# Optimization experiments

Hardware: AMD Instinct MI355X
Metric: run time of the kernel (lower is better)

Reference implementation:

```python
import jax, jax.numpy as jnp
import numpy as np


def setup_inputs() -> dict:
    key = jax.random.key(0)
    k1, k2 = jax.random.split(key)
    B, C, Tx, Ty, d = 16, 64, 128, 128, 768
    xs = jax.random.normal(k1, (B, Tx, d), dtype=jnp.float32)
    ys = jax.random.normal(k2, (B, C, Ty, d), dtype=jnp.float32)
    return {"xs": xs, "ys": ys}


def reference(xs, ys):
    """UnifiedRetriever HardAttention scoring.

    xs: (B, T_x, d) mention poly-code embeddings
    ys: (B, C, T_y, d) candidate entity poly-code embeddings
    returns: (B, C) scores
    Matches torch: matmul(xs, ys.reshape(B,-1,d).T).reshape(B,Tx,C,Ty).max(-1)[0].sum(1)
    """
    # (B, Tx, C, Ty) dot-product similarity scores
    scores = jnp.einsum("bxd,bcyd->bxcy", xs, ys)
    # max over candidate tokens, sum over mention tokens -> (B, C)
    return scores.max(axis=-1).sum(axis=1)
```

## Files before the change

kernel.cpp:

```cpp
#include <hip/hip_runtime.h>

#define NB 16
#define NC 64
#define TX 128
#define TY 128
#define DD 768
#define BK 32
#define NT (DD / BK)

typedef __bf16 bf16_t;
typedef __bf16 bf16x8 __attribute__((ext_vector_type(8)));
typedef __bf16 bf16x4 __attribute__((ext_vector_type(4)));
typedef float  f32x4  __attribute__((ext_vector_type(4)));

__device__ __forceinline__ unsigned swz(unsigned r, unsigned kb) {
  return r * 64u + ((((kb >> 4) & 3u) ^ ((r >> 1) & 3u)) << 4) + (kb & 15u);
}

__device__ __forceinline__ void cvt_store(void* dst, f32x4 v) {
  bf16x4 q;
  q[0] = (bf16_t)v[0]; q[1] = (bf16_t)v[1]; q[2] = (bf16_t)v[2]; q[3] = (bf16_t)v[3];
  *(bf16x4*)dst = q;
}

__global__ __launch_bounds__(256, 4) void ur_score_kernel(
    const float* __restrict__ xs, const float* __restrict__ ys,
    float* __restrict__ out)
{
  __shared__ char lds[2][2][8192];
  __shared__ float wsum[4];

  const int u  = blockIdx.x;
  const int b  = u & 15;
  const int c  = u >> 4;
  const int bc = b * NC + c;

  const int tid  = threadIdx.x;
  const int lane = tid & 63;
  const int w    = tid >> 6;

  const unsigned r0 = (unsigned)tid >> 3;
  const unsigned j0 = (unsigned)tid & 7u;
  const unsigned soff0 = swz(r0, j0 * 8u);
  const float* Ap = xs + (size_t)b  * TX * DD + r0 * DD + j0 * 4;
  const float* Bp = ys + (size_t)bc * TY * DD + r0 * DD + j0 * 4;

  f32x4 acc[2][8];
  #pragma unroll
  for (int m = 0; m < 2; ++m)
    #pragma unroll
    for (int n = 0; n < 8; ++n)
      #pragma unroll
      for (int k = 0; k < 4; ++k)
        acc[m][n][k] = 0.0f;

  f32x4 pa[4], pb[4];

  #pragma unroll
  for (int i = 0; i < 4; ++i) {
    pa[i] = __builtin_nontemporal_load((const f32x4*)(Ap + i * 32 * DD));
    pb[i] = __builtin_nontemporal_load((const f32x4*)(Bp + i * 32 * DD));
  }
  #pragma unroll
  for (int i = 0; i < 4; ++i) {
    cvt_store(&lds[0][0][soff0 + 2048u * i], pa[i]);
    cvt_store(&lds[0][1][soff0 + 2048u * i], pb[i]);
  }
  #pragma unroll
  for (int i = 0; i < 4; ++i) {
    pa[i] = __builtin_nontemporal_load((const f32x4*)(Ap + BK + i * 32 * DD));
    pb[i] = __builtin_nontemporal_load((const f32x4*)(Bp + BK + i * 32 * DD));
  }
  asm volatile("s_waitcnt lgkmcnt(0)" ::: "memory");
  __builtin_amdgcn_s_barrier();
  asm volatile("" ::: "memory");

  const unsigned kb = ((unsigned)lane >> 4) << 4;
  const unsigned rA = (unsigned)(w * 32 + (lane & 15));
  const unsigned rB = (unsigned)(lane & 15);
  const unsigned aoff = swz(rA, kb);
  const unsigned boff = swz(rB, kb);

  int cur = 0;
  for (int t = 0; t < NT; ++t) {
    if (t + 1 < NT) {
      #pragma unroll
      for (int i = 0; i < 4; ++i) {
        cvt_store(&lds[cur ^ 1][0][soff0 + 2048u * i], pa[i]);
        cvt_store(&lds[cur ^ 1][1][soff0 + 2048u * i], pb[i]);
      }
    }
    if (t + 2 < NT) {
      #pragma unroll
      for (int i = 0; i < 4; ++i) {
        pa[i] = __builtin_nontemporal_load((const f32x4*)(Ap + (t + 2) * BK + i * 32 * DD));
        pb[i] = __builtin_nontemporal_load((const f32x4*)(Bp + (t + 2) * BK + i * 32 * DD));
      }
    }
    bf16x8 af0 = *(const bf16x8*)&lds[cur][0][aoff];
    bf16x8 af1 = *(const bf16x8*)&lds[cur][0][aoff + 1024u];
    bf16x8 bfr[8];
    #pragma unroll
    for (int n = 0; n < 8; ++n)
      bfr[n] = *(const bf16x8*)&lds[cur][1][boff + 1024u * n];
    #pragma unroll
    for (int n = 0; n < 8; ++n)
      acc[0][n] = __builtin_amdgcn_mfma_f32_16x16x32_bf16(af0, bfr[n], acc[0][n], 0, 0, 0);
    #pragma unroll
    for (int n = 0; n < 8; ++n)
      acc[1][n] = __builtin_amdgcn_mfma_f32_16x16x32_bf16(af1, bfr[n], acc[1][n], 0, 0, 0);

    asm volatile("s_waitcnt lgkmcnt(0)" ::: "memory");
    __builtin_amdgcn_s_barrier();
    asm volatile("" ::: "memory");
    cur ^= 1;
  }

  float rm[2][4];
  #pragma unroll
  for (int m = 0; m < 2; ++m)
    #pragma unroll
    for (int i = 0; i < 4; ++i) {
      float v = acc[m][0][i];
      #pragma unroll
      for (int n = 1; n < 8; ++n) v = fmaxf(v, acc[m][n][i]);
      rm[m][i] = v;
    }
  #pragma unroll
  for (int mask = 1; mask < 16; mask <<= 1)
    #pragma unroll
    for (int m = 0; m < 2; ++m)
      #pragma unroll
      for (int i = 0; i < 4; ++i)
        rm[m][i] = fmaxf(rm[m][i], __shfl_xor(rm[m][i], mask, 64));

  float ps = 0.0f;
  #pragma unroll
  for (int m = 0; m < 2; ++m)
    #pragma unroll
    for (int i = 0; i < 4; ++i) ps += rm[m][i];
  ps += __shfl_xor(ps, 16, 64);
  ps += __shfl_xor(ps, 32, 64);

  if (lane == 0) wsum[w] = ps;
  __syncthreads();
  if (tid == 0) out[bc] = wsum[0] + wsum[1] + wsum[2] + wsum[3];
}

extern "C" void kernel_launch(void* const* d_in, const int* in_sizes, int n_in,
                              void* d_out, int out_size, void* d_ws, size_t ws_size,
                              hipStream_t stream) {
  const float* xs = (const float*)d_in[0];
  const float* ys = (const float*)d_in[1];
  float* out = (float*)d_out;
  ur_score_kernel<<<dim3(NB * NC), dim3(256), 0, stream>>>(xs, ys, out);
}
```

Before: 90.45 us.

## Double threads per block to 512 and switch xs loads to cached

Each block now uses 8 waves instead of 4, and each wave computes 16 rows of the 128x128 tile instead of 32. This halves the per-thread global loads and the accumulator registers, aiming for more latency hiding from additional resident waves. The xs loads drop the nontemporal hint so the shared mention embeddings can stay in cache across the 64 candidate blocks. The cost is more threads contending at each barrier, and every wave still reads all 8 B fragments, which raises LDS read traffic per MFMA.

```diff
diff --git a/kernel.cpp b/kernel.cpp
--- a/kernel.cpp
+++ b/kernel.cpp
@@ -23,12 +23,12 @@
   *(bf16x4*)dst = q;
 }
 
-__global__ __launch_bounds__(256, 4) void ur_score_kernel(
+__global__ __launch_bounds__(512, 2) void ur_score_kernel(
     const float* __restrict__ xs, const float* __restrict__ ys,
     float* __restrict__ out)
 {
   __shared__ char lds[2][2][8192];
-  __shared__ float wsum[4];
+  __shared__ float wsum[8];
 
   const int u  = blockIdx.x;
   const int b  = u & 15;
@@ -45,38 +45,36 @@
   const float* Ap = xs + (size_t)b  * TX * DD + r0 * DD + j0 * 4;
   const float* Bp = ys + (size_t)bc * TY * DD + r0 * DD + j0 * 4;
 
-  f32x4 acc[2][8];
+  f32x4 acc[8];
   #pragma unroll
-  for (int m = 0; m < 2; ++m)
+  for (int n = 0; n < 8; ++n)
     #pragma unroll
-    for (int n = 0; n < 8; ++n)
-      #pragma unroll
-      for (int k = 0; k < 4; ++k)
-        acc[m][n][k] = 0.0f;
+    for (int k = 0; k < 4; ++k)
+      acc[n][k] = 0.0f;
 
-  f32x4 pa[4], pb[4];
+  f32x4 pa[2], pb[2];
 
   #pragma unroll
-  for (int i = 0; i < 4; ++i) {
-    pa[i] = __builtin_nontemporal_load((const f32x4*)(Ap + i * 32 * DD));
-    pb[i] = __builtin_nontemporal_load((const f32x4*)(Bp + i * 32 * DD));
+  for (int i = 0; i < 2; ++i) {
+    pa[i] = *(const f32x4*)(Ap + i * 64 * DD);
+    pb[i] = __builtin_nontemporal_load((const f32x4*)(Bp + i * 64 * DD));
   }
   #pragma unroll
-  for (int i = 0; i < 4; ++i) {
-    cvt_store(&lds[0][0][soff0 + 2048u * i], pa[i]);
-    cvt_store(&lds[0][1][soff0 + 2048u * i], pb[i]);
+  for (int i = 0; i < 2; ++i) {
+    cvt_store(&lds[0][0][soff0 + 4096u * i], pa[i]);
+    cvt_store(&lds[0][1][soff0 + 4096u * i], pb[i]);
   }
   #pragma unroll
-  for (int i = 0; i < 4; ++i) {
-    pa[i] = __builtin_nontemporal_load((const f32x4*)(Ap + BK + i * 32 * DD));
-    pb[i] = __builtin_nontemporal_load((const f32x4*)(Bp + BK + i * 32 * DD));
+  for (int i = 0; i < 2; ++i) {
+    pa[i] = *(const f32x4*)(Ap + BK + i * 64 * DD);
+    pb[i] = __builtin_nontemporal_load((const f32x4*)(Bp + BK + i * 64 * DD));
   }
   asm volatile("s_waitcnt lgkmcnt(0)" ::: "memory");
   __builtin_amdgcn_s_barrier();
   asm volatile("" ::: "memory");
 
   const unsigned kb = ((unsigned)lane >> 4) << 4;
-  const unsigned rA = (unsigned)(w * 32 + (lane & 15));
+  const unsigned rA = (unsigned)(w * 16 + (lane & 15));
   const unsigned rB = (unsigned)(lane & 15);
   const unsigned aoff = swz(rA, kb);
   const unsigned boff = swz(rB, kb);
@@ -85,30 +83,26 @@
   for (int t = 0; t < NT; ++t) {
     if (t + 1 < NT) {
       #pragma unroll
-      for (int i = 0; i < 4; ++i) {
-        cvt_store(&lds[cur ^ 1][0][soff0 + 2048u * i], pa[i]);
-        cvt_store(&lds[cur ^ 1][1][soff0 + 2048u * i], pb[i]);
+      for (int i = 0; i < 2; ++i) {
+        cvt_store(&lds[cur ^ 1][0][soff0 + 4096u * i], pa[i]);
+        cvt_store(&lds[cur ^ 1][1][soff0 + 4096u * i], pb[i]);
       }
     }
     if (t + 2 < NT) {
       #pragma unroll
-      for (int i = 0; i < 4; ++i) {
-        pa[i] = __builtin_nontemporal_load((const f32x4*)(Ap + (t + 2) * BK + i * 32 * DD));
-        pb[i] = __builtin_nontemporal_load((const f32x4*)(Bp + (t + 2) * BK + i * 32 * DD));
+      for (int i = 0; i < 2; ++i) {
+        pa[i] = *(const f32x4*)(Ap + (t + 2) * BK + i * 64 * DD);
+        pb[i] = __builtin_nontemporal_load((const f32x4*)(Bp + (t + 2) * BK + i * 64 * DD));
       }
     }
-    bf16x8 af0 = *(const bf16x8*)&lds[cur][0][aoff];
-    bf16x8 af1 = *(const bf16x8*)&lds[cur][0][aoff + 1024u];
+    bf16x8 af = *(const bf16x8*)&lds[cur][0][aoff];
     bf16x8 bfr[8];
     #pragma unroll
     for (int n = 0; n < 8; ++n)
       bfr[n] = *(const bf16x8*)&lds[cur][1][boff + 1024u * n];
     #pragma unroll
     for (int n = 0; n < 8; ++n)
-      acc[0][n] = __builtin_amdgcn_mfma_f32_16x16x32_bf16(af0, bfr[n], acc[0][n], 0, 0, 0);
-    #pragma unroll
-    for (int n = 0; n < 8; ++n)
-      acc[1][n] = __builtin_amdgcn_mfma_f32_16x16x32_bf16(af1, bfr[n], acc[1][n], 0, 0, 0);
+      acc[n] = __builtin_amdgcn_mfma_f32_16x16x32_bf16(af, bfr[n], acc[n], 0, 0, 0);
 
     asm volatile("s_waitcnt lgkmcnt(0)" ::: "memory");
     __builtin_amdgcn_s_barrier();
@@ -116,35 +110,32 @@
     cur ^= 1;
   }
 
-  float rm[2][4];
+  float rm[4];
   #pragma unroll
-  for (int m = 0; m < 2; ++m)
+  for (int i = 0; i < 4; ++i) {
+    float v = acc[0][i];
     #pragma unroll
-    for (int i = 0; i < 4; ++i) {
-      float v = acc[m][0][i];
-      #pragma unroll
-      for (int n = 1; n < 8; ++n) v = fmaxf(v, acc[m][n][i]);
-      rm[m][i] = v;
-    }
+    for (int n = 1; n < 8; ++n) v = fmaxf(v, acc[n][i]);
+    rm[i] = v;
+  }
   #pragma unroll
   for (int mask = 1; mask < 16; mask <<= 1)
     #pragma unroll
-    for (int m = 0; m < 2; ++m)
-      #pragma unroll
-      for (int i = 0; i < 4; ++i)
-        rm[m][i] = fmaxf(rm[m][i], __shfl_xor(rm[m][i], mask, 64));
+    for (int i = 0; i < 4; ++i)
+      rm[i] = fmaxf(rm[i], __shfl_xor(rm[i], mask, 64));
 
-  float ps = 0.0f;
-  #pragma unroll
-  for (int m = 0; m < 2; ++m)
-    #pragma unroll
-    for (int i = 0; i < 4; ++i) ps += rm[m][i];
+  float ps = rm[0] + rm[1] + rm[2] + rm[3];
   ps += __shfl_xor(ps, 16, 64);
   ps += __shfl_xor(ps, 32, 64);
 
   if (lane == 0) wsum[w] = ps;
   __syncthreads();
-  if (tid == 0) out[bc] = wsum[0] + wsum[1] + wsum[2] + wsum[3];
+  if (tid == 0) {
+    float s = 0.0f;
+    #pragma unroll
+    for (int i = 0; i < 8; ++i) s += wsum[i];
+    out[bc] = s;
+  }
 }
 
 extern "C" void kernel_launch(void* const* d_in, const int* in_sizes, int n_in,
@@ -153,5 +144,5 @@
   const float* xs = (const float*)d_in[0];
   const float* ys = (const float*)d_in[1];
   float* out = (float*)d_out;
-  ur_score_kernel<<<dim3(NB * NC), dim3(256), 0, stream>>>(xs, ys, out);
+  ur_score_kernel<<<dim3(NB * NC), dim3(512), 0, stream>>>(xs, ys, out);
 }
```

Measured after the change: 81.99 us. 1.1x faster.
